# Kernel tuning notes

Measured on AMD Instinct MI355X. Metric: run time of the kernel, lower is better.

Reference implementation:

```python
import jax, jax.numpy as jnp
import numpy as np

C = 128      # hidden_channels
H = 4        # heads
DH = C // H
G = 4096     # num genes (segments)
R = 4096     # num reactions
E = 65536    # total (reaction, gene) pairs
LMAX = 64    # padded segment length
NB = 4       # blocks: 2 encoder SABs + 1 PMA + 1 decoder SAB
EPS = 1e-5


def _ln(x, g, b):
    m = jnp.mean(x, axis=-1, keepdims=True)
    v = jnp.mean((x - m) ** 2, axis=-1, keepdims=True)
    return (x - m) * jax.lax.rsqrt(v + EPS) * g + b


def setup_inputs() -> dict:
    key = jax.random.key(0)
    ks = jax.random.split(key, 12)
    sc = 1.0 / np.sqrt(C)
    zb = jnp.zeros((NB, C), jnp.float32)
    ob = jnp.ones((NB, C), jnp.float32)
    # every gene gets >= 1 reaction (matches realistic GEM mapping; avoids empty segments)
    gene_idx = jnp.sort(jnp.concatenate([
        jnp.arange(G, dtype=jnp.int32),
        jax.random.randint(ks[8], (E - G,), 0, G, jnp.int32)]))
    return {
        'reaction_features': jax.random.normal(ks[0], (R, C), jnp.float32),
        'Wq': jax.random.normal(ks[1], (NB, C, C), jnp.float32) * sc,
        'Wk': jax.random.normal(ks[2], (NB, C, C), jnp.float32) * sc,
        'Wv': jax.random.normal(ks[3], (NB, C, C), jnp.float32) * sc,
        'Wo': jax.random.normal(ks[4], (NB, C, C), jnp.float32) * sc,
        'bq': zb, 'bk': zb, 'bv': zb, 'bo': zb,
        'Wlin': jax.random.normal(ks[5], (NB, C, C), jnp.float32) * sc,
        'blin': zb,
        'g1': ob, 'b1': zb, 'g2': ob, 'b2': zb,
        'seed': jax.random.normal(ks[6], (1, 1, C), jnp.float32) * sc,
        'rxn_idx': jax.random.randint(ks[7], (E,), 0, R, jnp.int32),
        'gene_idx': gene_idx,
        'num_genes': G,
        'Lmax': LMAX,
    }


def _forward(reaction_features, Wq, Wk, Wv, Wo, bq, bk, bv, bo, Wlin, blin,
             g1, b1, g2, b2, seed, rxn_idx, gene_idx, num_genes, Lmax):
    E_ = gene_idx.shape[0]
    feats = reaction_features[rxn_idx]                      # [E, C] gather
    counts = jax.ops.segment_sum(jnp.ones((E_,), jnp.int32), gene_idx,
                                 num_segments=num_genes)
    starts = jnp.cumsum(counts) - counts                    # first flat index of each segment
    pos = jnp.arange(E_, dtype=jnp.int32) - starts[gene_idx]
    # to_dense_batch: [G, Lmax, C] + mask
    x = jnp.zeros((num_genes, Lmax, C), feats.dtype).at[gene_idx, pos].set(feats, mode='drop')
    mask = jnp.zeros((num_genes, Lmax), bool).at[gene_idx, pos].set(True, mode='drop')

    def mab(q_in, kv_in, q_mask, kv_mask, i):
        B, Lq, _ = q_in.shape
        Lk = kv_in.shape[1]
        q = (q_in @ Wq[i] + bq[i]).reshape(B, Lq, H, DH)
        k = (kv_in @ Wk[i] + bk[i]).reshape(B, Lk, H, DH)
        v = (kv_in @ Wv[i] + bv[i]).reshape(B, Lk, H, DH)
        scores = jnp.einsum('bqhd,bkhd->bhqk', q, k) / np.sqrt(DH)
        if kv_mask is not None:
            scores = jnp.where(kv_mask[:, None, None, :], scores, -1e30)
        a = jax.nn.softmax(scores, axis=-1)
        attn = jnp.einsum('bhqk,bkhd->bqhd', a, v).reshape(B, Lq, C) @ Wo[i] + bo[i]
        if q_mask is not None:
            attn = jnp.where(q_mask[:, :, None], attn, 0.0)
        out = _ln(attn + q_in, g1[i], b1[i])
        out = out + jax.nn.relu(out @ Wlin[i] + blin[i])
        return _ln(out, g2[i], b2[i])

    h = mab(x, x, mask, mask, 0)          # encoder SAB 1
    h = mab(h, h, mask, mask, 1)          # encoder SAB 2
    s = jnp.broadcast_to(seed, (num_genes, seed.shape[1], C))
    h = mab(s, h, None, mask, 2)          # PMA (1 seed point)
    h = mab(h, h, None, None, 3)          # decoder SAB
    h = jnp.nan_to_num(h)
    return h.reshape(num_genes, -1)       # [G, C] (concat over 1 seed)


def reference(reaction_features, Wq, Wk, Wv, Wo, bq, bk, bv, bo, Wlin, blin,
              g1, b1, g2, b2, seed, rxn_idx, gene_idx, num_genes, Lmax):
    return _forward(reaction_features, Wq, Wk, Wv, Wo, bq, bk, bv, bo, Wlin,
                    blin, g1, b1, g2, b2, seed, rxn_idx, gene_idx, num_genes, Lmax)
```

## Files before the change

kernel.cpp:

```cpp
#include <hip/hip_runtime.h>
#include <hip/hip_bf16.h>
#include <math.h>

#define C 128
#define H 4
#define LMAX 64
#define EPS 1e-5f
#define ISQ 0.17677669529663687f

using short8  = __attribute__((ext_vector_type(8))) short;
using short4v = __attribute__((ext_vector_type(4))) short;
using f32x4   = __attribute__((ext_vector_type(4))) float;

__device__ __forceinline__ float wsum(float v){
  #pragma unroll
  for (int o = 32; o > 0; o >>= 1) v += __shfl_xor(v, o, 64);
  return v;
}
__device__ __forceinline__ float wmax(float v){
  #pragma unroll
  for (int o = 32; o > 0; o >>= 1) v = fmaxf(v, __shfl_xor(v, o, 64));
  return v;
}
__device__ __forceinline__ short f2bs(float f){
  __hip_bfloat16 b = __float2bfloat16(f);
  union { __hip_bfloat16 b; short u; } cv; cv.b = b; return cv.u;
}
__device__ __forceinline__ float b2f(short u){
  return __uint_as_float(((unsigned)(unsigned short)u) << 16);
}

__global__ void prep_wfrag(const float* __restrict__ Wq, const float* __restrict__ Wk,
                           const float* __restrict__ Wv, const float* __restrict__ Wo,
                           const float* __restrict__ Wlin, short* __restrict__ wf){
  int bid = blockIdx.x, l = threadIdx.x;
  int tile = bid & 31, mb = bid >> 5;
  int mat = mb >> 2, blk = mb & 3;
  const float* W = (mat==0?Wq : mat==1?Wk : mat==2?Wv : mat==3?Wo : Wlin) + blk*C*C;
  int nt = tile >> 2, kt = tile & 3;
  int col = nt*16 + (l & 15);
  int k0  = kt*32 + ((l >> 4) << 3);
  short8 v;
  #pragma unroll
  for (int j = 0; j < 8; j++) v[j] = f2bs(W[(k0 + j)*C + col]);
  *(short8*)(wf + ((size_t)mb*32 + tile)*512 + (size_t)l*8) = v;
}

__global__ void prep_qrow(const float* __restrict__ seed, const float* __restrict__ Wq,
                          const float* __restrict__ bq, float* __restrict__ qrow){
  int t = threadIdx.x;
  const float* wq2 = Wq + 2*C*C;
  float acc = bq[2*C + t];
  #pragma unroll 4
  for (int k = 0; k < C; k++) acc = fmaf(seed[k], wq2[k*C + t], acc);
  qrow[t] = acc;
}

__global__ void seg_kernel(const int* __restrict__ gidx, int E, int G,
                           int* __restrict__ starts, int* __restrict__ counts,
                           int* __restrict__ cnt, int* __restrict__ gcr){
  int g = blockIdx.x * blockDim.x + threadIdx.x;
  if (g >= G) return;
  int lo = 0, hi = E;
  while (lo < hi){ int m = (lo + hi) >> 1; if (gidx[m] < g) lo = m + 1; else hi = m; }
  int s = lo; hi = E;
  while (lo < hi){ int m = (lo + hi) >> 1; if (gidx[m] < g + 1) lo = m + 1; else hi = m; }
  starts[g] = s;
  int c_ = lo - s; counts[g] = c_;
  int L = c_ > LMAX ? LMAX : c_; if (L < 1) L = 1;
  int cl = (L - 1) >> 4;
  int r = atomicAdd(&cnt[cl], 1);
  gcr[g] = (cl << 28) | r;
}

__global__ void fill_kernel(int G, const int* __restrict__ cnt, const int* __restrict__ gcr,
                            int* __restrict__ binfo, int* __restrict__ nbins){
  int g = blockIdx.x * blockDim.x + threadIdx.x;
  if (g >= G) return;
  int nb1 = (cnt[0] + 3) >> 2, nb2 = (cnt[1] + 1) >> 1, nb3 = cnt[2];
  if (g == 0) *nbins = nb1 + nb2 + nb3 + cnt[3];
  int v = gcr[g]; int cl = v >> 28; int r = v & 0x0FFFFFFF;
  int bin, slot;
  if      (cl == 0){ bin = r >> 2;             slot = r & 3; }
  else if (cl == 1){ bin = nb1 + (r >> 1);     slot = (r & 1) * 2; }
  else if (cl == 2){ bin = nb1 + nb2 + r;      slot = 0; }
  else             { bin = nb1 + nb2 + nb3 + r; slot = 0; }
  binfo[bin*4 + slot] = g;
}

__device__ __forceinline__ f32x4 mfma4(short8 a0, short8 a1, short8 a2, short8 a3,
                                       const short* __restrict__ wf, int nt, int l){
  f32x4 acc = {0.f, 0.f, 0.f, 0.f};
  acc = __builtin_amdgcn_mfma_f32_16x16x32_bf16(a0, *(const short8*)(wf + ((nt*4+0)*64 + l)*8), acc, 0,0,0);
  acc = __builtin_amdgcn_mfma_f32_16x16x32_bf16(a1, *(const short8*)(wf + ((nt*4+1)*64 + l)*8), acc, 0,0,0);
  acc = __builtin_amdgcn_mfma_f32_16x16x32_bf16(a2, *(const short8*)(wf + ((nt*4+2)*64 + l)*8), acc, 0,0,0);
  acc = __builtin_amdgcn_mfma_f32_16x16x32_bf16(a3, *(const short8*)(wf + ((nt*4+3)*64 + l)*8), acc, 0,0,0);
  return acc;
}

__device__ __forceinline__ void ln_rows(const short (*src)[136], short (*dst)[136],
                                        const float* __restrict__ gg,
                                        const float* __restrict__ bb, int t){
  int row = t >> 2, q4 = t & 3;
  float v[32];
  float sm = 0.f;
  #pragma unroll
  for (int kk = 0; kk < 32; ++kk){
    float x = b2f(src[row][q4*32 + kk]);
    v[kk] = x; sm += x;
  }
  sm += __shfl_xor(sm, 1);
  sm += __shfl_xor(sm, 2);
  float mean = sm * (1.f/128.f);
  float s2 = 0.f;
  #pragma unroll
  for (int kk = 0; kk < 32; ++kk){ float d = v[kk] - mean; s2 += d*d; }
  s2 += __shfl_xor(s2, 1);
  s2 += __shfl_xor(s2, 2);
  float rs = rsqrtf(s2*(1.f/128.f) + EPS);
  #pragma unroll
  for (int kk = 0; kk < 32; ++kk){
    int col = q4*32 + kk;
    dst[row][col] = f2bs((v[kk] - mean)*rs*gg[col] + bb[col]);
  }
}

__global__ __launch_bounds__(256, 2) void gene_bin_kernel(
  const float* __restrict__ RF, const short* __restrict__ wfrag,
  const float* __restrict__ qrow,
  const float* __restrict__ bq, const float* __restrict__ bk,
  const float* __restrict__ bv, const float* __restrict__ bo,
  const float* __restrict__ blin,
  const float* __restrict__ g1, const float* __restrict__ b1,
  const float* __restrict__ g2, const float* __restrict__ b2,
  const int* __restrict__ rxn_idx, const int* __restrict__ starts,
  const int* __restrict__ counts, const int* __restrict__ binfo,
  const int* __restrict__ meta, float* __restrict__ pooled)
{
  if ((int)blockIdx.x >= meta[0]) return;
  __shared__ short xb[64][136];
  __shared__ short qb[64][136];
  __shared__ short kb[64][136];
  __shared__ short vt[128][72];
  __shared__ __align__(16) short sc[64][72];
  __shared__ float qrl[C];
  __shared__ int mg[4], mL[4], ms0[4], mbase[4];

  const int bin = blockIdx.x;
  const int t = threadIdx.x, w = t >> 6, l = t & 63;
  const int hi = l >> 4, c = l & 15;

  if (t == 0){
    int s = 0;
    while (s < 4){
      int g = binfo[bin*4 + s];
      if (g >= 0){
        int Lg = counts[g]; if (Lg > LMAX) Lg = LMAX;
        int ntg = (Lg + 15) >> 4;
        for (int u = 0; u < ntg; ++u){ mg[s+u] = g; mL[s+u] = Lg; ms0[s+u] = starts[g]; mbase[s+u] = s; }
        s += ntg;
      } else { mg[s] = -1; mL[s] = 0; ms0[s] = 0; mbase[s] = s; s++; }
    }
  }
  if (t < C) qrl[t] = qrow[t];
  __syncthreads();

  for (int idx = t; idx < 64*16; idx += 256){
    int row = idx >> 4, ch = idx & 15;
    int s = row >> 4;
    int g = mg[s];
    int ro = row - mbase[s]*16;
    short8 u = {0,0,0,0,0,0,0,0};
    if (g >= 0 && ro < mL[s]){
      int rr = rxn_idx[ms0[s] + ro];
      const float* src = RF + (size_t)rr*C + ch*8;
      float4 v0 = *(const float4*)(src);
      float4 v1 = *(const float4*)(src + 4);
      u[0]=f2bs(v0.x); u[1]=f2bs(v0.y); u[2]=f2bs(v0.z); u[3]=f2bs(v0.w);
      u[4]=f2bs(v1.x); u[5]=f2bs(v1.y); u[6]=f2bs(v1.z); u[7]=f2bs(v1.w);
    }
    *(short8*)&xb[row][ch*8] = u;
  }
  {
    short8 z = {0,0,0,0,0,0,0,0};
    for (int idx = t; idx < 64*9; idx += 256){
      int row = idx / 9, ch = idx - row*9;
      *(short8*)&sc[row][ch*8] = z;
    }
  }
  __syncthreads();

  for (int blk = 0; blk < 2; ++blk){
    {
      short8 ax[4][4];
      #pragma unroll
      for (int mt = 0; mt < 4; ++mt)
        #pragma unroll
        for (int kk = 0; kk < 4; ++kk)
          ax[mt][kk] = *(const short8*)&xb[mt*16 + c][kk*32 + hi*8];
      #pragma unroll
      for (int i = 0; i < 6; ++i){
        int pr = w + 4*i;
        int mat = pr >> 3, nt = pr & 7;
        const short* wfm = wfrag + (size_t)(mat*4 + blk)*16384;
        const float* bias = (mat == 0 ? bq : mat == 1 ? bk : bv);
        int col = nt*16 + c;
        float bb = bias[blk*C + col];
        #pragma unroll
        for (int mt = 0; mt < 4; ++mt){
          f32x4 acc = mfma4(ax[mt][0], ax[mt][1], ax[mt][2], ax[mt][3], wfm, nt, l);
          if (mat == 2){
            short4v pk;
            #pragma unroll
            for (int r = 0; r < 4; r++) pk[r] = f2bs(acc[r] + bb);
            *(short4v*)&vt[col][mt*16 + hi*4] = pk;
          } else if (mat == 0){
            #pragma unroll
            for (int r = 0; r < 4; r++) qb[mt*16 + hi*4 + r][col] = f2bs(acc[r] + bb);
          } else {
            #pragma unroll
            for (int r = 0; r < 4; r++) kb[mt*16 + hi*4 + r][col] = f2bs(acc[r] + bb);
          }
        }
      }
    }
    __syncthreads();

    for (int h = 0; h < H; ++h){
      for (int idx = w; idx < 16; idx += 4){
        int mt = idx >> 2, kt = idx & 3;
        int gm = mg[mt];
        if (gm >= 0 && gm == mg[kt]){
          short8 a = *(const short8*)&qb[mt*16 + c][h*32 + hi*8];
          short8 b = *(const short8*)&kb[kt*16 + c][h*32 + hi*8];
          f32x4 acc = {0.f, 0.f, 0.f, 0.f};
          acc = __builtin_amdgcn_mfma_f32_16x16x32_bf16(a, b, acc, 0,0,0);
          #pragma unroll
          for (int r = 0; r < 4; r++) sc[mt*16 + hi*4 + r][kt*16 + c] = f2bs(acc[r] * ISQ);
        }
      }
      __syncthreads();
      {
        int row = t >> 2, q4 = t & 3;
        int s = row >> 4;
        if (mg[s] >= 0){
          int kbeg = mbase[s]*16;
          int kend = kbeg + mL[s];
          int send = kbeg + (((mL[s] + 15) >> 4) << 4);
          int b0 = q4*16;
          float e[16];
          float mx = -3.4e38f;
          #pragma unroll
          for (int kk = 0; kk < 16; ++kk){
            int col = b0 + kk;
            bool ok = (col >= kbeg) && (col < kend);
            float lg = ok ? b2f(sc[row][col]) : -3.4e38f;
            e[kk] = lg;
            mx = fmaxf(mx, lg);
          }
          mx = fmaxf(mx, __shfl_xor(mx, 1));
          mx = fmaxf(mx, __shfl_xor(mx, 2));
          float sm = 0.f;
          #pragma unroll
          for (int kk = 0; kk < 16; ++kk){
            int col = b0 + kk;
            bool ok = (col >= kbeg) && (col < kend);
            float ee = ok ? __expf(e[kk] - mx) : 0.f;
            e[kk] = ee; sm += ee;
          }
          sm += __shfl_xor(sm, 1);
          sm += __shfl_xor(sm, 2);
          float inv = 1.f / sm;
          #pragma unroll
          for (int kk = 0; kk < 16; ++kk){
            int col = b0 + kk;
            if (col >= kbeg && col < send)
              sc[row][col] = f2bs((col < kend) ? e[kk]*inv : 0.f);
          }
        }
      }
      __syncthreads();
      for (int idx = w; idx < 8; idx += 4){
        int mt = idx >> 1, dt = idx & 1;
        if (mg[mt] >= 0){
          f32x4 acc = {0.f, 0.f, 0.f, 0.f};
          #pragma unroll
          for (int ks = 0; ks < 2; ++ks){
            short8 a = *(const short8*)&sc[mt*16 + c][ks*32 + hi*8];
            short8 b = *(const short8*)&vt[h*32 + dt*16 + c][ks*32 + hi*8];
            acc = __builtin_amdgcn_mfma_f32_16x16x32_bf16(a, b, acc, 0,0,0);
          }
          int col = h*32 + dt*16 + c;
          #pragma unroll
          for (int r = 0; r < 4; r++) qb[mt*16 + hi*4 + r][col] = f2bs(acc[r]);
        }
      }
      __syncthreads();
    }

    {
      short8 aw[4];
      #pragma unroll
      for (int kk = 0; kk < 4; kk++) aw[kk] = *(const short8*)&qb[w*16 + c][kk*32 + hi*8];
      const short* wfo = wfrag + (size_t)(3*4 + blk)*16384;
      #pragma unroll 2
      for (int nt = 0; nt < 8; ++nt){
        int col = nt*16 + c;
        f32x4 acc = mfma4(aw[0], aw[1], aw[2], aw[3], wfo, nt, l);
        float bb = bo[blk*C + col];
        #pragma unroll
        for (int r = 0; r < 4; r++){
          int row = w*16 + hi*4 + r;
          xb[row][col] = f2bs(acc[r] + bb + b2f(xb[row][col]));
        }
      }
    }
    __syncthreads();
    ln_rows(xb, xb, g1 + blk*C, b1 + blk*C, t);
    __syncthreads();

    {
      short8 aw[4];
      #pragma unroll
      for (int kk = 0; kk < 4; kk++) aw[kk] = *(const short8*)&xb[w*16 + c][kk*32 + hi*8];
      const short* wfl = wfrag + (size_t)(4*4 + blk)*16384;
      #pragma unroll 2
      for (int nt = 0; nt < 8; ++nt){
        int col = nt*16 + c;
        f32x4 acc = mfma4(aw[0], aw[1], aw[2], aw[3], wfl, nt, l);
        float bb = blin[blk*C + col];
        #pragma unroll
        for (int r = 0; r < 4; r++){
          int row = w*16 + hi*4 + r;
          kb[row][col] = f2bs(b2f(xb[row][col]) + fmaxf(acc[r] + bb, 0.f));
        }
      }
    }
    __syncthreads();
    ln_rows(kb, xb, g2 + blk*C, b2 + blk*C, t);
    __syncthreads();
  }

  {
    short8 aw[4];
    #pragma unroll
    for (int kk = 0; kk < 4; kk++) aw[kk] = *(const short8*)&xb[w*16 + c][kk*32 + hi*8];
    const short* wfk2 = wfrag + (size_t)(1*4 + 2)*16384;
    const short* wfv2 = wfrag + (size_t)(2*4 + 2)*16384;
    #pragma unroll 2
    for (int nt = 0; nt < 8; ++nt){
      int col = nt*16 + c;
      f32x4 acc = mfma4(aw[0], aw[1], aw[2], aw[3], wfk2, nt, l);
      float bb = bk[2*C + col];
      #pragma unroll
      for (int r = 0; r < 4; r++) kb[w*16 + hi*4 + r][col] = f2bs(acc[r] + bb);
      acc = mfma4(aw[0], aw[1], aw[2], aw[3], wfv2, nt, l);
      bb = bv[2*C + col];
      short4v pk;
      #pragma unroll
      for (int r = 0; r < 4; r++) pk[r] = f2bs(acc[r] + bb);
      *(short4v*)&vt[col][w*16 + hi*4] = pk;
    }
  }
  __syncthreads();
  {
    int g = mg[w];
    if (g >= 0 && mbase[w] == w){
      int L = mL[w];
      int row = w*16 + l;
      float* ps = (float*)&sc[0][0];
      #pragma unroll
      for (int h = 0; h < 4; ++h){
        float a = -3.4e38f;
        if (l < L){
          float acc = 0.f;
          #pragma unroll 8
          for (int dd = 0; dd < 32; ++dd)
            acc = fmaf(b2f(kb[row][h*32 + dd]), qrl[h*32 + dd], acc);
          a = acc * ISQ;
        }
        float mx = wmax(a);
        float e = (l < L) ? __expf(a - mx) : 0.f;
        float s = wsum(e);
        ps[(w*4 + h)*64 + l] = e / s;
      }
      #pragma unroll
      for (int half = 0; half < 2; ++half){
        int d = l + half*64;
        int h = d >> 5;
        float acc = 0.f;
        for (int kk = 0; kk < L; ++kk)
          acc = fmaf(ps[(w*4 + h)*64 + kk], b2f(vt[d][w*16 + kk]), acc);
        pooled[(size_t)g*C + d] = acc;
      }
    }
  }
}

__global__ __launch_bounds__(256) void tail_kernel(
  const float* __restrict__ pooled,
  const float* __restrict__ Wv, const float* __restrict__ Wo,
  const float* __restrict__ Wlin,
  const float* __restrict__ bv, const float* __restrict__ bo,
  const float* __restrict__ blin,
  const float* __restrict__ g1, const float* __restrict__ b1,
  const float* __restrict__ g2, const float* __restrict__ b2,
  const float* __restrict__ seed, float* __restrict__ out)
{
  __shared__ float row0[C], row1[C], row2[C];
  const int g = blockIdx.x, t = threadIdx.x, w = t >> 6, l = t & 63;
  if (t < C) row1[t] = pooled[(size_t)g*C + t];
  __syncthreads();
  if (t < C){
    float acc = bo[2*C + t];
    const float* wo2 = Wo + 2*C*C;
    #pragma unroll 4
    for (int k = 0; k < C; k++) acc = fmaf(row1[k], wo2[k*C + t], acc);
    row0[t] = acc + seed[t];
  }
  __syncthreads();
  if (w == 0){
    float v0 = row0[l], v1 = row0[l + 64];
    float m = wsum(v0 + v1) * (1.f / C);
    float d0 = v0 - m, d1 = v1 - m;
    float va = wsum(d0*d0 + d1*d1) * (1.f / C);
    float rs = rsqrtf(va + EPS);
    row0[l]      = d0 * rs * g1[2*C + l]      + b1[2*C + l];
    row0[l + 64] = d1 * rs * g1[2*C + l + 64] + b1[2*C + l + 64];
  }
  __syncthreads();
  if (t < C){
    float acc = blin[2*C + t];
    const float* wl2 = Wlin + 2*C*C;
    #pragma unroll 4
    for (int k = 0; k < C; k++) acc = fmaf(row0[k], wl2[k*C + t], acc);
    row1[t] = row0[t] + fmaxf(acc, 0.f);
  }
  __syncthreads();
  if (w == 0){
    float v0 = row1[l], v1 = row1[l + 64];
    float m = wsum(v0 + v1) * (1.f / C);
    float d0 = v0 - m, d1 = v1 - m;
    float va = wsum(d0*d0 + d1*d1) * (1.f / C);
    float rs = rsqrtf(va + EPS);
    row0[l]      = d0 * rs * g2[2*C + l]      + b2[2*C + l];
    row0[l + 64] = d1 * rs * g2[2*C + l + 64] + b2[2*C + l + 64];
  }
  __syncthreads();
  {
    const float* wv3 = Wv + 3*C*C; const float* wo3 = Wo + 3*C*C; const float* wl3 = Wlin + 3*C*C;
    if (t < C){
      float acc = bv[3*C + t];
      #pragma unroll 4
      for (int k = 0; k < C; k++) acc = fmaf(row0[k], wv3[k*C + t], acc);
      row1[t] = acc;
    }
    __syncthreads();
    if (t < C){
      float acc = bo[3*C + t];
      #pragma unroll 4
      for (int k = 0; k < C; k++) acc = fmaf(row1[k], wo3[k*C + t], acc);
      row2[t] = acc + row0[t];
    }
    __syncthreads();
    if (w == 0){
      float v0 = row2[l], v1 = row2[l + 64];
      float m = wsum(v0 + v1) * (1.f / C);
      float d0 = v0 - m, d1 = v1 - m;
      float va = wsum(d0*d0 + d1*d1) * (1.f / C);
      float rs = rsqrtf(va + EPS);
      row2[l]      = d0 * rs * g1[3*C + l]      + b1[3*C + l];
      row2[l + 64] = d1 * rs * g1[3*C + l + 64] + b1[3*C + l + 64];
    }
    __syncthreads();
    if (t < C){
      float acc = blin[3*C + t];
      #pragma unroll 4
      for (int k = 0; k < C; k++) acc = fmaf(row2[k], wl3[k*C + t], acc);
      row1[t] = row2[t] + fmaxf(acc, 0.f);
    }
    __syncthreads();
    if (w == 0){
      float v0 = row1[l], v1 = row1[l + 64];
      float m = wsum(v0 + v1) * (1.f / C);
      float d0 = v0 - m, d1 = v1 - m;
      float va = wsum(d0*d0 + d1*d1) * (1.f / C);
      float rs = rsqrtf(va + EPS);
      float r0 = d0 * rs * g2[3*C + l]      + b2[3*C + l];
      float r1 = d1 * rs * g2[3*C + l + 64] + b2[3*C + l + 64];
      if (isnan(r0)) r0 = 0.f; else if (isinf(r0)) r0 = r0 > 0 ? 3.402823466e38f : -3.402823466e38f;
      if (isnan(r1)) r1 = 0.f; else if (isinf(r1)) r1 = r1 > 0 ? 3.402823466e38f : -3.402823466e38f;
      out[(size_t)g*C + l]      = r0;
      out[(size_t)g*C + l + 64] = r1;
    }
  }
}

extern "C" void kernel_launch(void* const* d_in, const int* in_sizes, int n_in,
                              void* d_out, int out_size, void* d_ws, size_t ws_size,
                              hipStream_t stream){
  const float* RF   = (const float*)d_in[0];
  const float* Wq   = (const float*)d_in[1];
  const float* Wk   = (const float*)d_in[2];
  const float* Wv   = (const float*)d_in[3];
  const float* Wo   = (const float*)d_in[4];
  const float* bq   = (const float*)d_in[5];
  const float* bk   = (const float*)d_in[6];
  const float* bv   = (const float*)d_in[7];
  const float* bo   = (const float*)d_in[8];
  const float* Wlin = (const float*)d_in[9];
  const float* blin = (const float*)d_in[10];
  const float* g1   = (const float*)d_in[11];
  const float* b1   = (const float*)d_in[12];
  const float* g2   = (const float*)d_in[13];
  const float* b2   = (const float*)d_in[14];
  const float* seed = (const float*)d_in[15];
  const int* rxn    = (const int*)d_in[16];
  const int* gidx   = (const int*)d_in[17];

  int E = in_sizes[16];
  int G = out_size / C;

  char* base = (char*)d_ws;
  short* wfrag = (short*)base;
  float* qrow  = (float*)(base + 655360);
  int*   meta  = (int*)(base + 655872);
  int*   starts= (int*)(base + 655936);
  int*   counts= (int*)(base + 655936 + (size_t)4*G);
  int*   gcr   = (int*)(base + 655936 + (size_t)8*G);
  int*   binfo = (int*)(base + 655936 + (size_t)12*G);
  float* pooled= (float*)(base + 655936 + (size_t)28*G);

  hipMemsetAsync(meta, 0, 64, stream);
  hipMemsetAsync(binfo, 0xFF, (size_t)16*G, stream);
  prep_wfrag<<<640, 64, 0, stream>>>(Wq, Wk, Wv, Wo, Wlin, wfrag);
  prep_qrow<<<1, 128, 0, stream>>>(seed, Wq, bq, qrow);
  seg_kernel<<<(G + 255)/256, 256, 0, stream>>>(gidx, E, G, starts, counts, meta + 1, gcr);
  fill_kernel<<<(G + 255)/256, 256, 0, stream>>>(G, meta + 1, gcr, binfo, meta);
  gene_bin_kernel<<<G, 256, 0, stream>>>(RF, wfrag, qrow, bq, bk, bv, bo, blin,
      g1, b1, g2, b2, rxn, starts, counts, binfo, meta, pooled);
  tail_kernel<<<G, 256, 0, stream>>>(pooled, Wv, Wo, Wlin, bv, bo, blin,
      g1, b1, g2, b2, seed, (float*)d_out);
}
```

Baseline: 310.1 us.

## Batch 16 genes per block in tail kernel to reuse weight loads

The tail kernel now handles 16 genes per block instead of one. Each thread computes one output column for 8 rows, so every weight element loaded from memory is reused across 8 rows, and all 256 threads take part instead of 128. LayerNorm uses 16-lane shuffles, one row per 16-thread group. This cuts weight traffic per gene by a factor of about 16, at the cost of more registers and shared memory and fewer blocks (256 instead of 4096).

```diff
diff --git a/kernel.cpp b/kernel.cpp
--- a/kernel.cpp
+++ b/kernel.cpp
@@ -397,6 +397,36 @@
   }
 }
 
+__device__ __forceinline__ void gemmf(const float (*src)[132], const float* __restrict__ W,
+                                      float (&o)[8], int col, int rg){
+  #pragma unroll
+  for (int r = 0; r < 8; ++r) o[r] = 0.f;
+  #pragma unroll 4
+  for (int k = 0; k < 128; ++k){
+    float wv = W[k*C + col];
+    #pragma unroll
+    for (int r = 0; r < 8; ++r) o[r] = fmaf(src[rg*8 + r][k], wv, o[r]);
+  }
+}
+
+__device__ __forceinline__ void ln16f(float (*buf)[132], const float* __restrict__ gg,
+                                      const float* __restrict__ bb, int t){
+  int row = t >> 4, cg = t & 15;
+  float v[8]; float s = 0.f;
+  #pragma unroll
+  for (int k = 0; k < 8; ++k){ v[k] = buf[row][cg*8 + k]; s += v[k]; }
+  s += __shfl_xor(s,1); s += __shfl_xor(s,2); s += __shfl_xor(s,4); s += __shfl_xor(s,8);
+  float mean = s * (1.f/128.f);
+  float q = 0.f;
+  #pragma unroll
+  for (int k = 0; k < 8; ++k){ float d = v[k] - mean; q += d*d; }
+  q += __shfl_xor(q,1); q += __shfl_xor(q,2); q += __shfl_xor(q,4); q += __shfl_xor(q,8);
+  float rs = rsqrtf(q*(1.f/128.f) + EPS);
+  #pragma unroll
+  for (int k = 0; k < 8; ++k)
+    buf[row][cg*8 + k] = (v[k] - mean)*rs*gg[cg*8 + k] + bb[cg*8 + k];
+}
+
 __global__ __launch_bounds__(256) void tail_kernel(
   const float* __restrict__ pooled,
   const float* __restrict__ Wv, const float* __restrict__ Wo,
@@ -405,93 +435,80 @@
   const float* __restrict__ blin,
   const float* __restrict__ g1, const float* __restrict__ b1,
   const float* __restrict__ g2, const float* __restrict__ b2,
-  const float* __restrict__ seed, float* __restrict__ out)
+  const float* __restrict__ seed, float* __restrict__ out, int G)
 {
-  __shared__ float row0[C], row1[C], row2[C];
-  const int g = blockIdx.x, t = threadIdx.x, w = t >> 6, l = t & 63;
-  if (t < C) row1[t] = pooled[(size_t)g*C + t];
-  __syncthreads();
-  if (t < C){
-    float acc = bo[2*C + t];
-    const float* wo2 = Wo + 2*C*C;
-    #pragma unroll 4
-    for (int k = 0; k < C; k++) acc = fmaf(row1[k], wo2[k*C + t], acc);
-    row0[t] = acc + seed[t];
-  }
-  __syncthreads();
-  if (w == 0){
-    float v0 = row0[l], v1 = row0[l + 64];
-    float m = wsum(v0 + v1) * (1.f / C);
-    float d0 = v0 - m, d1 = v1 - m;
-    float va = wsum(d0*d0 + d1*d1) * (1.f / C);
-    float rs = rsqrtf(va + EPS);
-    row0[l]      = d0 * rs * g1[2*C + l]      + b1[2*C + l];
-    row0[l + 64] = d1 * rs * g1[2*C + l + 64] + b1[2*C + l + 64];
-  }
-  __syncthreads();
-  if (t < C){
-    float acc = blin[2*C + t];
-    const float* wl2 = Wlin + 2*C*C;
-    #pragma unroll 4
-    for (int k = 0; k < C; k++) acc = fmaf(row0[k], wl2[k*C + t], acc);
-    row1[t] = row0[t] + fmaxf(acc, 0.f);
-  }
-  __syncthreads();
-  if (w == 0){
-    float v0 = row1[l], v1 = row1[l + 64];
-    float m = wsum(v0 + v1) * (1.f / C);
-    float d0 = v0 - m, d1 = v1 - m;
-    float va = wsum(d0*d0 + d1*d1) * (1.f / C);
-    float rs = rsqrtf(va + EPS);
-    row0[l]      = d0 * rs * g2[2*C + l]      + b2[2*C + l];
-    row0[l + 64] = d1 * rs * g2[2*C + l + 64] + b2[2*C + l + 64];
-  }
-  __syncthreads();
-  {
-    const float* wv3 = Wv + 3*C*C; const float* wo3 = Wo + 3*C*C; const float* wl3 = Wlin + 3*C*C;
-    if (t < C){
-      float acc = bv[3*C + t];
-      #pragma unroll 4
-      for (int k = 0; k < C; k++) acc = fmaf(row0[k], wv3[k*C + t], acc);
-      row1[t] = acc;
-    }
-    __syncthreads();
-    if (t < C){
-      float acc = bo[3*C + t];
-      #pragma unroll 4
-      for (int k = 0; k < C; k++) acc = fmaf(row1[k], wo3[k*C + t], acc);
-      row2[t] = acc + row0[t];
-    }
-    __syncthreads();
-    if (w == 0){
-      float v0 = row2[l], v1 = row2[l + 64];
-      float m = wsum(v0 + v1) * (1.f / C);
-      float d0 = v0 - m, d1 = v1 - m;
-      float va = wsum(d0*d0 + d1*d1) * (1.f / C);
-      float rs = rsqrtf(va + EPS);
-      row2[l]      = d0 * rs * g1[3*C + l]      + b1[3*C + l];
-      row2[l + 64] = d1 * rs * g1[3*C + l + 64] + b1[3*C + l + 64];
-    }
-    __syncthreads();
-    if (t < C){
-      float acc = blin[3*C + t];
-      #pragma unroll 4
-      for (int k = 0; k < C; k++) acc = fmaf(row2[k], wl3[k*C + t], acc);
-      row1[t] = row2[t] + fmaxf(acc, 0.f);
-    }
-    __syncthreads();
-    if (w == 0){
-      float v0 = row1[l], v1 = row1[l + 64];
-      float m = wsum(v0 + v1) * (1.f / C);
-      float d0 = v0 - m, d1 = v1 - m;
-      float va = wsum(d0*d0 + d1*d1) * (1.f / C);
-      float rs = rsqrtf(va + EPS);
-      float r0 = d0 * rs * g2[3*C + l]      + b2[3*C + l];
-      float r1 = d1 * rs * g2[3*C + l + 64] + b2[3*C + l + 64];
-      if (isnan(r0)) r0 = 0.f; else if (isinf(r0)) r0 = r0 > 0 ? 3.402823466e38f : -3.402823466e38f;
-      if (isnan(r1)) r1 = 0.f; else if (isinf(r1)) r1 = r1 > 0 ? 3.402823466e38f : -3.402823466e38f;
-      out[(size_t)g*C + l]      = r0;
-      out[(size_t)g*C + l + 64] = r1;
+  __shared__ float ta[16][132];
+  __shared__ float tb[16][132];
+  const int t = threadIdx.x;
+  const int g0 = blockIdx.x * 16;
+  const int col = t & 127, rg = t >> 7;
+  float o[8], res[8];
+
+  {
+    int row = t >> 4, ch = t & 15;
+    float4 v0 = {0,0,0,0}, v1 = {0,0,0,0};
+    if (g0 + row < G){
+      const float* src = pooled + (size_t)(g0 + row)*C + ch*8;
+      v0 = *(const float4*)(src);
+      v1 = *(const float4*)(src + 4);
+    }
+    *(float4*)&ta[row][ch*8] = v0;
+    *(float4*)&ta[row][ch*8 + 4] = v1;
+  }
+  __syncthreads();
+
+  gemmf(ta, Wo + 2*C*C, o, col, rg);
+  {
+    float ss = seed[col], bb = bo[2*C + col];
+    #pragma unroll
+    for (int r = 0; r < 8; ++r) tb[rg*8 + r][col] = o[r] + bb + ss;
+  }
+  __syncthreads();
+  ln16f(tb, g1 + 2*C, b1 + 2*C, t);
+  __syncthreads();
+  gemmf(tb, Wlin + 2*C*C, o, col, rg);
+  {
+    float bb = blin[2*C + col];
+    #pragma unroll
+    for (int r = 0; r < 8; ++r) ta[rg*8 + r][col] = tb[rg*8 + r][col] + fmaxf(o[r] + bb, 0.f);
+  }
+  __syncthreads();
+  ln16f(ta, g2 + 2*C, b2 + 2*C, t);
+  __syncthreads();
+  gemmf(ta, Wv + 3*C*C, o, col, rg);
+  {
+    float bb = bv[3*C + col];
+    #pragma unroll
+    for (int r = 0; r < 8; ++r) tb[rg*8 + r][col] = o[r] + bb;
+  }
+  __syncthreads();
+  gemmf(tb, Wo + 3*C*C, o, col, rg);
+  {
+    float bb = bo[3*C + col];
+    #pragma unroll
+    for (int r = 0; r < 8; ++r) res[r] = ta[rg*8 + r][col];
+    #pragma unroll
+    for (int r = 0; r < 8; ++r) ta[rg*8 + r][col] = o[r] + bb + res[r];
+  }
+  __syncthreads();
+  ln16f(ta, g1 + 3*C, b1 + 3*C, t);
+  __syncthreads();
+  gemmf(ta, Wlin + 3*C*C, o, col, rg);
+  {
+    float bb = blin[3*C + col];
+    #pragma unroll
+    for (int r = 0; r < 8; ++r) tb[rg*8 + r][col] = ta[rg*8 + r][col] + fmaxf(o[r] + bb, 0.f);
+  }
+  __syncthreads();
+  ln16f(tb, g2 + 3*C, b2 + 3*C, t);
+  __syncthreads();
+  for (int idx = t; idx < 16*128; idx += 256){
+    int row = idx >> 7, cc = idx & 127;
+    if (g0 + row < G){
+      float v = tb[row][cc];
+      if (isnan(v)) v = 0.f;
+      else if (isinf(v)) v = v > 0 ? 3.402823466e38f : -3.402823466e38f;
+      out[(size_t)(g0 + row)*C + cc] = v;
     }
   }
 }
@@ -539,6 +556,6 @@
   fill_kernel<<<(G + 255)/256, 256, 0, stream>>>(G, meta + 1, gcr, binfo, meta);
   gene_bin_kernel<<<G, 256, 0, stream>>>(RF, wfrag, qrow, bq, bk, bv, bo, blin,
       g1, b1, g2, b2, rxn, starts, counts, binfo, meta, pooled);
-  tail_kernel<<<G, 256, 0, stream>>>(pooled, Wv, Wo, Wlin, bv, bo, blin,
-      g1, b1, g2, b2, seed, (float*)d_out);
-}
+  tail_kernel<<<(G + 15)/16, 256, 0, stream>>>(pooled, Wv, Wo, Wlin, bv, bo, blin,
+      g1, b1, g2, b2, seed, (float*)d_out, G);
+}
```

Measured after the change: 289.6 us. 6.6% less time.

## Fuse per-gene tail MLP into bin kernel and drop attention barriers

Applied to the files above, without the earlier changes.

Folds the separate tail kernel (PMA output projection, LN, FFN, decoder SAB) into the end of the gene-bin kernel. Each wave now runs the per-gene tail on its own pooled row, staged through the freed kb shared buffer. This removes one launch, the pooled round trip through global memory, and a 256-thread block per gene that mostly idled. The attention score and PV stages are reassigned so each wave owns its own 16-row tile, which lets several __syncthreads be dropped. The risk is that the remaining cross-wave reads (softmax rows, ln_rows reading xb after the Wo/Wlin writes) depend on wave-local row ownership and could race. The tail matvecs also run serially per wave, which lengthens the bin kernel.

```diff
diff --git a/kernel.cpp b/kernel.cpp
--- a/kernel.cpp
+++ b/kernel.cpp
@@ -128,6 +128,8 @@
 __global__ __launch_bounds__(256, 2) void gene_bin_kernel(
   const float* __restrict__ RF, const short* __restrict__ wfrag,
   const float* __restrict__ qrow,
+  const float* __restrict__ Wv, const float* __restrict__ Wo,
+  const float* __restrict__ Wlin, const float* __restrict__ seed,
   const float* __restrict__ bq, const float* __restrict__ bk,
   const float* __restrict__ bv, const float* __restrict__ bo,
   const float* __restrict__ blin,
@@ -135,7 +137,7 @@
   const float* __restrict__ g2, const float* __restrict__ b2,
   const int* __restrict__ rxn_idx, const int* __restrict__ starts,
   const int* __restrict__ counts, const int* __restrict__ binfo,
-  const int* __restrict__ meta, float* __restrict__ pooled)
+  const int* __restrict__ meta, float* __restrict__ out)
 {
   if ((int)blockIdx.x >= meta[0]) return;
   __shared__ short xb[64][136];
@@ -189,6 +191,8 @@
     }
   }
   __syncthreads();
+
+  const int myg = mg[w];
 
   for (int blk = 0; blk < 2; ++blk){
     {
@@ -227,19 +231,19 @@
     __syncthreads();
 
     for (int h = 0; h < H; ++h){
-      for (int idx = w; idx < 16; idx += 4){
-        int mt = idx >> 2, kt = idx & 3;
-        int gm = mg[mt];
-        if (gm >= 0 && gm == mg[kt]){
-          short8 a = *(const short8*)&qb[mt*16 + c][h*32 + hi*8];
-          short8 b = *(const short8*)&kb[kt*16 + c][h*32 + hi*8];
-          f32x4 acc = {0.f, 0.f, 0.f, 0.f};
-          acc = __builtin_amdgcn_mfma_f32_16x16x32_bf16(a, b, acc, 0,0,0);
-          #pragma unroll
-          for (int r = 0; r < 4; r++) sc[mt*16 + hi*4 + r][kt*16 + c] = f2bs(acc[r] * ISQ);
-        }
-      }
-      __syncthreads();
+      if (myg >= 0){
+        short8 a = *(const short8*)&qb[w*16 + c][h*32 + hi*8];
+        #pragma unroll
+        for (int kt = 0; kt < 4; ++kt){
+          if (mg[kt] == myg){
+            short8 b = *(const short8*)&kb[kt*16 + c][h*32 + hi*8];
+            f32x4 acc = {0.f, 0.f, 0.f, 0.f};
+            acc = __builtin_amdgcn_mfma_f32_16x16x32_bf16(a, b, acc, 0,0,0);
+            #pragma unroll
+            for (int r = 0; r < 4; r++) sc[w*16 + hi*4 + r][kt*16 + c] = f2bs(acc[r] * ISQ);
+          }
+        }
+      }
       {
         int row = t >> 2, q4 = t & 3;
         int s = row >> 4;
@@ -279,23 +283,21 @@
           }
         }
       }
-      __syncthreads();
-      for (int idx = w; idx < 8; idx += 4){
-        int mt = idx >> 1, dt = idx & 1;
-        if (mg[mt] >= 0){
+      if (myg >= 0){
+        #pragma unroll
+        for (int dt = 0; dt < 2; ++dt){
           f32x4 acc = {0.f, 0.f, 0.f, 0.f};
           #pragma unroll
           for (int ks = 0; ks < 2; ++ks){
-            short8 a = *(const short8*)&sc[mt*16 + c][ks*32 + hi*8];
+            short8 a = *(const short8*)&sc[w*16 + c][ks*32 + hi*8];
             short8 b = *(const short8*)&vt[h*32 + dt*16 + c][ks*32 + hi*8];
             acc = __builtin_amdgcn_mfma_f32_16x16x32_bf16(a, b, acc, 0,0,0);
           }
           int col = h*32 + dt*16 + c;
           #pragma unroll
-          for (int r = 0; r < 4; r++) qb[mt*16 + hi*4 + r][col] = f2bs(acc[r]);
-        }
-      }
-      __syncthreads();
+          for (int r = 0; r < 4; r++) qb[w*16 + hi*4 + r][col] = f2bs(acc[r]);
+        }
+      }
     }
 
     {
@@ -315,7 +317,6 @@
         }
       }
     }
-    __syncthreads();
     ln_rows(xb, xb, g1 + blk*C, b1 + blk*C, t);
     __syncthreads();
 
@@ -336,7 +337,6 @@
         }
       }
     }
-    __syncthreads();
     ln_rows(kb, xb, g2 + blk*C, b2 + blk*C, t);
     __syncthreads();
   }
@@ -363,6 +363,7 @@
     }
   }
   __syncthreads();
+
   {
     int g = mg[w];
     if (g >= 0 && mbase[w] == w){
@@ -384,114 +385,126 @@
         float s = wsum(e);
         ps[(w*4 + h)*64 + l] = e / s;
       }
-      #pragma unroll
-      for (int half = 0; half < 2; ++half){
-        int d = l + half*64;
-        int h = d >> 5;
+      float p0, p1;
+      {
+        int h0 = l >> 5;
         float acc = 0.f;
         for (int kk = 0; kk < L; ++kk)
-          acc = fmaf(ps[(w*4 + h)*64 + kk], b2f(vt[d][w*16 + kk]), acc);
-        pooled[(size_t)g*C + d] = acc;
-      }
-    }
-  }
-}
-
-__global__ __launch_bounds__(256) void tail_kernel(
-  const float* __restrict__ pooled,
-  const float* __restrict__ Wv, const float* __restrict__ Wo,
-  const float* __restrict__ Wlin,
-  const float* __restrict__ bv, const float* __restrict__ bo,
-  const float* __restrict__ blin,
-  const float* __restrict__ g1, const float* __restrict__ b1,
-  const float* __restrict__ g2, const float* __restrict__ b2,
-  const float* __restrict__ seed, float* __restrict__ out)
-{
-  __shared__ float row0[C], row1[C], row2[C];
-  const int g = blockIdx.x, t = threadIdx.x, w = t >> 6, l = t & 63;
-  if (t < C) row1[t] = pooled[(size_t)g*C + t];
-  __syncthreads();
-  if (t < C){
-    float acc = bo[2*C + t];
-    const float* wo2 = Wo + 2*C*C;
-    #pragma unroll 4
-    for (int k = 0; k < C; k++) acc = fmaf(row1[k], wo2[k*C + t], acc);
-    row0[t] = acc + seed[t];
-  }
-  __syncthreads();
-  if (w == 0){
-    float v0 = row0[l], v1 = row0[l + 64];
-    float m = wsum(v0 + v1) * (1.f / C);
-    float d0 = v0 - m, d1 = v1 - m;
-    float va = wsum(d0*d0 + d1*d1) * (1.f / C);
-    float rs = rsqrtf(va + EPS);
-    row0[l]      = d0 * rs * g1[2*C + l]      + b1[2*C + l];
-    row0[l + 64] = d1 * rs * g1[2*C + l + 64] + b1[2*C + l + 64];
-  }
-  __syncthreads();
-  if (t < C){
-    float acc = blin[2*C + t];
-    const float* wl2 = Wlin + 2*C*C;
-    #pragma unroll 4
-    for (int k = 0; k < C; k++) acc = fmaf(row0[k], wl2[k*C + t], acc);
-    row1[t] = row0[t] + fmaxf(acc, 0.f);
-  }
-  __syncthreads();
-  if (w == 0){
-    float v0 = row1[l], v1 = row1[l + 64];
-    float m = wsum(v0 + v1) * (1.f / C);
-    float d0 = v0 - m, d1 = v1 - m;
-    float va = wsum(d0*d0 + d1*d1) * (1.f / C);
-    float rs = rsqrtf(va + EPS);
-    row0[l]      = d0 * rs * g2[2*C + l]      + b2[2*C + l];
-    row0[l + 64] = d1 * rs * g2[2*C + l + 64] + b2[2*C + l + 64];
-  }
-  __syncthreads();
-  {
-    const float* wv3 = Wv + 3*C*C; const float* wo3 = Wo + 3*C*C; const float* wl3 = Wlin + 3*C*C;
-    if (t < C){
-      float acc = bv[3*C + t];
-      #pragma unroll 4
-      for (int k = 0; k < C; k++) acc = fmaf(row0[k], wv3[k*C + t], acc);
-      row1[t] = acc;
-    }
-    __syncthreads();
-    if (t < C){
-      float acc = bo[3*C + t];
-      #pragma unroll 4
-      for (int k = 0; k < C; k++) acc = fmaf(row1[k], wo3[k*C + t], acc);
-      row2[t] = acc + row0[t];
-    }
-    __syncthreads();
-    if (w == 0){
-      float v0 = row2[l], v1 = row2[l + 64];
-      float m = wsum(v0 + v1) * (1.f / C);
-      float d0 = v0 - m, d1 = v1 - m;
-      float va = wsum(d0*d0 + d1*d1) * (1.f / C);
-      float rs = rsqrtf(va + EPS);
-      row2[l]      = d0 * rs * g1[3*C + l]      + b1[3*C + l];
-      row2[l + 64] = d1 * rs * g1[3*C + l + 64] + b1[3*C + l + 64];
-    }
-    __syncthreads();
-    if (t < C){
-      float acc = blin[3*C + t];
-      #pragma unroll 4
-      for (int k = 0; k < C; k++) acc = fmaf(row2[k], wl3[k*C + t], acc);
-      row1[t] = row2[t] + fmaxf(acc, 0.f);
-    }
-    __syncthreads();
-    if (w == 0){
-      float v0 = row1[l], v1 = row1[l + 64];
-      float m = wsum(v0 + v1) * (1.f / C);
-      float d0 = v0 - m, d1 = v1 - m;
-      float va = wsum(d0*d0 + d1*d1) * (1.f / C);
-      float rs = rsqrtf(va + EPS);
-      float r0 = d0 * rs * g2[3*C + l]      + b2[3*C + l];
-      float r1 = d1 * rs * g2[3*C + l + 64] + b2[3*C + l + 64];
-      if (isnan(r0)) r0 = 0.f; else if (isinf(r0)) r0 = r0 > 0 ? 3.402823466e38f : -3.402823466e38f;
-      if (isnan(r1)) r1 = 0.f; else if (isinf(r1)) r1 = r1 > 0 ? 3.402823466e38f : -3.402823466e38f;
-      out[(size_t)g*C + l]      = r0;
-      out[(size_t)g*C + l + 64] = r1;
+          acc = fmaf(ps[(w*4 + h0)*64 + kk], b2f(vt[l][w*16 + kk]), acc);
+        p0 = acc;
+        int d1 = l + 64, h1 = d1 >> 5;
+        acc = 0.f;
+        for (int kk = 0; kk < L; ++kk)
+          acc = fmaf(ps[(w*4 + h1)*64 + kk], b2f(vt[d1][w*16 + kk]), acc);
+        p1 = acc;
+      }
+
+      float* fs  = (float*)&kb[w*16][0];
+      float* fsA = fs;
+      float* fsB = fs + 128;
+      float* fsC = fs + 256;
+      float o0, o1;
+
+      fsB[l] = p0; fsB[64 + l] = p1;
+      {
+        const float* Wm = Wo + 2*C*C;
+        o0 = bo[2*C + l]; o1 = bo[2*C + 64 + l];
+        #pragma unroll 4
+        for (int k = 0; k < C; ++k){
+          float x = fsB[k];
+          o0 = fmaf(x, Wm[k*C + l], o0);
+          o1 = fmaf(x, Wm[k*C + 64 + l], o1);
+        }
+        fsA[l]      = o0 + seed[l];
+        fsA[64 + l] = o1 + seed[64 + l];
+      }
+      {
+        float v0 = fsA[l], v1 = fsA[64 + l];
+        float m = wsum(v0 + v1) * (1.f / C);
+        float d0 = v0 - m, d1 = v1 - m;
+        float va = wsum(d0*d0 + d1*d1) * (1.f / C);
+        float rs = rsqrtf(va + EPS);
+        fsA[l]      = d0 * rs * g1[2*C + l]      + b1[2*C + l];
+        fsA[64 + l] = d1 * rs * g1[2*C + 64 + l] + b1[2*C + 64 + l];
+      }
+      {
+        const float* Wm = Wlin + 2*C*C;
+        o0 = blin[2*C + l]; o1 = blin[2*C + 64 + l];
+        #pragma unroll 4
+        for (int k = 0; k < C; ++k){
+          float x = fsA[k];
+          o0 = fmaf(x, Wm[k*C + l], o0);
+          o1 = fmaf(x, Wm[k*C + 64 + l], o1);
+        }
+        fsB[l]      = fsA[l]      + fmaxf(o0, 0.f);
+        fsB[64 + l] = fsA[64 + l] + fmaxf(o1, 0.f);
+      }
+      {
+        float v0 = fsB[l], v1 = fsB[64 + l];
+        float m = wsum(v0 + v1) * (1.f / C);
+        float d0 = v0 - m, d1 = v1 - m;
+        float va = wsum(d0*d0 + d1*d1) * (1.f / C);
+        float rs = rsqrtf(va + EPS);
+        fsA[l]      = d0 * rs * g2[2*C + l]      + b2[2*C + l];
+        fsA[64 + l] = d1 * rs * g2[2*C + 64 + l] + b2[2*C + 64 + l];
+      }
+      {
+        const float* Wm = Wv + 3*C*C;
+        o0 = bv[3*C + l]; o1 = bv[3*C + 64 + l];
+        #pragma unroll 4
+        for (int k = 0; k < C; ++k){
+          float x = fsA[k];
+          o0 = fmaf(x, Wm[k*C + l], o0);
+          o1 = fmaf(x, Wm[k*C + 64 + l], o1);
+        }
+        fsB[l] = o0; fsB[64 + l] = o1;
+      }
+      {
+        const float* Wm = Wo + 3*C*C;
+        o0 = bo[3*C + l]; o1 = bo[3*C + 64 + l];
+        #pragma unroll 4
+        for (int k = 0; k < C; ++k){
+          float x = fsB[k];
+          o0 = fmaf(x, Wm[k*C + l], o0);
+          o1 = fmaf(x, Wm[k*C + 64 + l], o1);
+        }
+        fsC[l]      = o0 + fsA[l];
+        fsC[64 + l] = o1 + fsA[64 + l];
+      }
+      {
+        float v0 = fsC[l], v1 = fsC[64 + l];
+        float m = wsum(v0 + v1) * (1.f / C);
+        float d0 = v0 - m, d1 = v1 - m;
+        float va = wsum(d0*d0 + d1*d1) * (1.f / C);
+        float rs = rsqrtf(va + EPS);
+        fsC[l]      = d0 * rs * g1[3*C + l]      + b1[3*C + l];
+        fsC[64 + l] = d1 * rs * g1[3*C + 64 + l] + b1[3*C + 64 + l];
+      }
+      {
+        const float* Wm = Wlin + 3*C*C;
+        o0 = blin[3*C + l]; o1 = blin[3*C + 64 + l];
+        #pragma unroll 4
+        for (int k = 0; k < C; ++k){
+          float x = fsC[k];
+          o0 = fmaf(x, Wm[k*C + l], o0);
+          o1 = fmaf(x, Wm[k*C + 64 + l], o1);
+        }
+        fsB[l]      = fsC[l]      + fmaxf(o0, 0.f);
+        fsB[64 + l] = fsC[64 + l] + fmaxf(o1, 0.f);
+      }
+      {
+        float v0 = fsB[l], v1 = fsB[64 + l];
+        float m = wsum(v0 + v1) * (1.f / C);
+        float d0 = v0 - m, d1 = v1 - m;
+        float va = wsum(d0*d0 + d1*d1) * (1.f / C);
+        float rs = rsqrtf(va + EPS);
+        float r0 = d0 * rs * g2[3*C + l]      + b2[3*C + l];
+        float r1 = d1 * rs * g2[3*C + 64 + l] + b2[3*C + 64 + l];
+        if (isnan(r0)) r0 = 0.f; else if (isinf(r0)) r0 = r0 > 0 ? 3.402823466e38f : -3.402823466e38f;
+        if (isnan(r1)) r1 = 0.f; else if (isinf(r1)) r1 = r1 > 0 ? 3.402823466e38f : -3.402823466e38f;
+        out[(size_t)g*C + l]      = r0;
+        out[(size_t)g*C + 64 + l] = r1;
+      }
     }
   }
 }
@@ -529,7 +542,6 @@
   int*   counts= (int*)(base + 655936 + (size_t)4*G);
   int*   gcr   = (int*)(base + 655936 + (size_t)8*G);
   int*   binfo = (int*)(base + 655936 + (size_t)12*G);
-  float* pooled= (float*)(base + 655936 + (size_t)28*G);
 
   hipMemsetAsync(meta, 0, 64, stream);
   hipMemsetAsync(binfo, 0xFF, (size_t)16*G, stream);
@@ -537,8 +549,7 @@
   prep_qrow<<<1, 128, 0, stream>>>(seed, Wq, bq, qrow);
   seg_kernel<<<(G + 255)/256, 256, 0, stream>>>(gidx, E, G, starts, counts, meta + 1, gcr);
   fill_kernel<<<(G + 255)/256, 256, 0, stream>>>(G, meta + 1, gcr, binfo, meta);
-  gene_bin_kernel<<<G, 256, 0, stream>>>(RF, wfrag, qrow, bq, bk, bv, bo, blin,
-      g1, b1, g2, b2, rxn, starts, counts, binfo, meta, pooled);
-  tail_kernel<<<G, 256, 0, stream>>>(pooled, Wv, Wo, Wlin, bv, bo, blin,
-      g1, b1, g2, b2, seed, (float*)d_out);
-}
+  gene_bin_kernel<<<G, 256, 0, stream>>>(RF, wfrag, qrow, Wv, Wo, Wlin, seed,
+      bq, bk, bv, bo, blin, g1, b1, g2, b2, rxn, starts, counts, binfo, meta,
+      (float*)d_out);
+}
```

New measurement: 308.0 us. About the same (-0.7%).
